# Kernel optimization log

Hardware: AMD Instinct MI355X
Metric: run time of the kernel (lower is better)

Reference implementation:

```python
import jax, jax.numpy as jnp
import numpy as np

E = 128      # embedding_dim
H = 64       # hidden_dim
B = 2048     # batch
L = 200      # history length
NEG = -1e30  # stand-in for -inf (avoids NaN for all-pad rows; same math when any key unmasked)


def setup_inputs() -> dict:
    key = jax.random.key(0)
    ks = jax.random.split(key, 10)
    s1 = 1.0 / np.sqrt(4 * E)
    s2 = 1.0 / np.sqrt(H)
    return {
        "query": jax.random.normal(ks[0], (B, E), jnp.float32),
        "keys": jax.random.normal(ks[1], (B, L, E), jnp.float32),
        "mask": jax.random.randint(ks[2], (B, L), 0, 2, jnp.int32),
        "W1": jax.random.uniform(ks[3], (4 * E, H), jnp.float32, -s1, s1),
        "b1": jax.random.uniform(ks[4], (H,), jnp.float32, -s1, s1),
        "W2": jax.random.uniform(ks[5], (H, H), jnp.float32, -s2, s2),
        "b2": jax.random.uniform(ks[6], (H,), jnp.float32, -s2, s2),
        "W3": jax.random.uniform(ks[7], (H, 1), jnp.float32, -s2, s2),
        "b3": jax.random.uniform(ks[8], (1,), jnp.float32, -s2, s2),
        "no_hist": jax.random.normal(ks[9], (E,), jnp.float32) * 0.001,
    }


def reference(query, keys, mask, W1, b1, W2, b2, W3, b3, no_hist):
    # q expanded over L, 4-way concat features: [q, k, q*k, q-k] -> (B, L, 4E)
    q = jnp.broadcast_to(query[:, None, :], keys.shape)
    attn_in = jnp.concatenate([q, keys, q * keys, q - keys], axis=-1)
    # 3-layer MLP scorer -> (B, L)
    h = jax.nn.relu(attn_in @ W1 + b1)
    h = jax.nn.relu(h @ W2 + b2)
    scores = (h @ W3 + b3)[..., 0]
    # masked softmax over L, then zero masked slots and renormalize
    m = mask.astype(scores.dtype)
    scores = jnp.where(m == 0, NEG, scores)
    attn = jax.nn.softmax(scores, axis=1) * m
    denom = jnp.sum(attn, axis=1, keepdims=True)
    attn = attn / (denom + 1e-12)
    # weighted sum of keys -> (B, E)
    user_interest = jnp.einsum("bl,ble->be", attn, keys)
    # rows with no history get the learned no-hist embedding
    all_pad = jnp.sum(m, axis=1) == 0  # (B,)
    user_interest = jnp.where(all_pad[:, None], no_hist[None, :], user_interest)
    return user_interest
```

## Files before the change

### kernel.cpp

```cpp
#include <hip/hip_runtime.h>


#define NB 2048
#define LE 128
#define LH 64
#define LL 200
#define NMT 13

typedef short bf16x8 __attribute__((ext_vector_type(8)));
typedef float f32x4 __attribute__((ext_vector_type(4)));

__device__ __forceinline__ short f2bf(float f) {
  unsigned u = __float_as_uint(f);
  u += 0x7fffu + ((u >> 16) & 1u);
  return (short)(u >> 16);
}

struct __align__(16) SM {
  short keys[208 * 128];
  short h1[4][16 * 72];
  float scores[208];
  float q[128];
  float bias1[64];
  float b2s[64];
  float w3s[64];
  float red[16];
};

__global__ void k0_prep(const float* __restrict__ W1, const float* __restrict__ W2,
                        float* __restrict__ BD, float* __restrict__ Cq,
                        float* __restrict__ AD, short* __restrict__ W2T) {
  int idx = blockIdx.x * 256 + threadIdx.x;
  if (idx < 8192) {
    int h = idx >> 7, e = idx & 127;
    BD[idx] = W1[(128 + e) * LH + h] - W1[(384 + e) * LH + h];
    Cq[idx] = W1[(256 + e) * LH + h];
    int e2 = idx >> 6, h2 = idx & 63;
    AD[idx] = W1[e2 * LH + h2] + W1[(384 + e2) * LH + h2];
    if (idx < 4096) {
      int c = idx >> 6, k = idx & 63;
      W2T[idx] = f2bf(W2[k * LH + c]);
    }
  }
}

__global__ void __launch_bounds__(256, 2)
din_attn(const float* __restrict__ query, const float* __restrict__ keysg,
         const int* __restrict__ mask, const float* __restrict__ b1,
         const float* __restrict__ b2, const float* __restrict__ W3,
         const float* __restrict__ no_hist,
         const float* __restrict__ BD, const float* __restrict__ Cq,
         const float* __restrict__ AD, const short* __restrict__ W2T,
         float* __restrict__ out)
{
  __shared__ SM sm;
  const int b    = blockIdx.x;
  const int t    = threadIdx.x;
  const int lane = t & 63;
  const int wv   = t >> 6;
  const int col  = lane & 15;
  const int quad = lane >> 4;

  int my_mask = 0;
  if (t < LL) my_mask = mask[b * LL + t];
  if (t < LE) sm.q[t] = query[b * LE + t];
  if (t < LH) { sm.b2s[t] = b2[t]; sm.w3s[t] = W3[t]; }
  __syncthreads();

  bf16x8 fB2[4][2];
  #pragma unroll
  for (int n = 0; n < 4; ++n)
    #pragma unroll
    for (int k2 = 0; k2 < 2; ++k2)
      fB2[n][k2] = *(const bf16x8*)&W2T[(n * 16 + col) * 64 + k2 * 32 + quad * 8];

  short* scratch = &sm.keys[0];
  #pragma unroll
  for (int i = 0; i < 4; ++i) {
    int idx = (t + 256 * i) * 8;
    int h = idx >> 7, e0 = idx & 127;
    float4 bd0 = *(const float4*)&BD[idx];
    float4 bd1 = *(const float4*)&BD[idx + 4];
    float4 c0  = *(const float4*)&Cq[idx];
    float4 c1  = *(const float4*)&Cq[idx + 4];
    bf16x8 w;
    w[0] = f2bf(bd0.x + sm.q[e0 + 0] * c0.x);
    w[1] = f2bf(bd0.y + sm.q[e0 + 1] * c0.y);
    w[2] = f2bf(bd0.z + sm.q[e0 + 2] * c0.z);
    w[3] = f2bf(bd0.w + sm.q[e0 + 3] * c0.w);
    w[4] = f2bf(bd1.x + sm.q[e0 + 4] * c1.x);
    w[5] = f2bf(bd1.y + sm.q[e0 + 5] * c1.y);
    w[6] = f2bf(bd1.z + sm.q[e0 + 6] * c1.z);
    w[7] = f2bf(bd1.w + sm.q[e0 + 7] * c1.w);
    *(bf16x8*)&scratch[h * 136 + e0] = w;
  }
  {
    int h = lane;
    float acc = 0.f;
    #pragma unroll 8
    for (int e = wv * 32; e < wv * 32 + 32; ++e)
      acc = fmaf(sm.q[e], AD[e * LH + h], acc);
    float* biasp = (float*)&sm.h1[0][0];
    biasp[wv * 64 + h] = acc;
  }
  __syncthreads();

  bf16x8 fB1[4][4];
  #pragma unroll
  for (int n = 0; n < 4; ++n)
    #pragma unroll
    for (int kt = 0; kt < 4; ++kt)
      fB1[n][kt] = *(const bf16x8*)&scratch[(n * 16 + col) * 136 + kt * 32 + quad * 8];

  if (t < LH) {
    const float* biasp = (const float*)&sm.h1[0][0];
    sm.bias1[t] = b1[t] + biasp[t] + biasp[64 + t] + biasp[128 + t] + biasp[192 + t];
  }
  __syncthreads();

  const float* kb = keysg + (size_t)b * LL * LE;
  short* h1w = &sm.h1[wv][0];

  auto do_tile = [&](int mt) {
    int row = mt * 16 + col;
    int rowg = row < LL ? row : LL - 1;
    const float* rp = kb + rowg * LE;
    bf16x8 a[4];
    #pragma unroll
    for (int kt = 0; kt < 4; ++kt) {
      float4 v0 = *(const float4*)&rp[kt * 32 + quad * 8];
      float4 v1 = *(const float4*)&rp[kt * 32 + quad * 8 + 4];
      bf16x8 av;
      av[0] = f2bf(v0.x); av[1] = f2bf(v0.y); av[2] = f2bf(v0.z); av[3] = f2bf(v0.w);
      av[4] = f2bf(v1.x); av[5] = f2bf(v1.y); av[6] = f2bf(v1.z); av[7] = f2bf(v1.w);
      a[kt] = av;
      *(bf16x8*)&sm.keys[row * 128 + (((kt * 4 + quad) ^ col) * 8)] = av;
    }
    #pragma unroll
    for (int n = 0; n < 4; ++n) {
      f32x4 acc = {0.f, 0.f, 0.f, 0.f};
      #pragma unroll
      for (int kt = 0; kt < 4; ++kt)
        acc = __builtin_amdgcn_mfma_f32_16x16x32_bf16(a[kt], fB1[n][kt], acc, 0, 0, 0);
      float bias = sm.bias1[n * 16 + col];
      #pragma unroll
      for (int i = 0; i < 4; ++i)
        h1w[(quad * 4 + i) * 72 + n * 16 + col] = f2bf(fmaxf(acc[i] + bias, 0.f));
    }
    bf16x8 a2[2];
    #pragma unroll
    for (int k2 = 0; k2 < 2; ++k2)
      a2[k2] = *(const bf16x8*)&h1w[col * 72 + k2 * 32 + quad * 8];
    float p[4] = {0.f, 0.f, 0.f, 0.f};
    #pragma unroll
    for (int n = 0; n < 4; ++n) {
      f32x4 c2 = {0.f, 0.f, 0.f, 0.f};
      c2 = __builtin_amdgcn_mfma_f32_16x16x32_bf16(a2[0], fB2[n][0], c2, 0, 0, 0);
      c2 = __builtin_amdgcn_mfma_f32_16x16x32_bf16(a2[1], fB2[n][1], c2, 0, 0, 0);
      float bb = sm.b2s[n * 16 + col];
      float w3 = sm.w3s[n * 16 + col];
      #pragma unroll
      for (int i = 0; i < 4; ++i)
        p[i] = fmaf(fmaxf(c2[i] + bb, 0.f), w3, p[i]);
    }
    #pragma unroll
    for (int i = 0; i < 4; ++i) {
      #pragma unroll
      for (int off = 1; off < 16; off <<= 1)
        p[i] += __shfl_xor(p[i], off);
      if (col == 0) sm.scores[mt * 16 + quad * 4 + i] = p[i];
    }
  };

  do_tile(wv);
  do_tile(wv + 4);
  do_tile(wv + 8);
  if (wv == 0) do_tile(12);
  __syncthreads();

  float sc = (t < LL) ? sm.scores[t] : -3.0e38f;
  float vmax = (my_mask != 0) ? sc : -3.0e38f;
  #pragma unroll
  for (int off = 1; off < 64; off <<= 1) vmax = fmaxf(vmax, __shfl_xor(vmax, off));
  if (lane == 0) sm.red[wv] = vmax;
  __syncthreads();
  float M = fmaxf(fmaxf(sm.red[0], sm.red[1]), fmaxf(sm.red[2], sm.red[3]));
  float ex = (t < LL && my_mask != 0) ? __expf(sc - M) : 0.f;
  float vsum = ex;
  #pragma unroll
  for (int off = 1; off < 64; off <<= 1) vsum += __shfl_xor(vsum, off);
  if (lane == 0) sm.red[4 + wv] = vsum;
  __syncthreads();
  float Z = sm.red[4] + sm.red[5] + sm.red[6] + sm.red[7];
  bool allpad = !(Z > 0.f);
  float rz = allpad ? 0.f : (1.f / Z);
  if (t < 208) sm.scores[t] = (t < LL) ? ex * rz : 0.f;
  __syncthreads();

  {
    const int part = t >> 5;
    const int ei = (t & 31) * 4;
    float a0 = 0.f, a1 = 0.f, a2s = 0.f, a3 = 0.f;
    int l0 = part * 25;
    #pragma unroll 5
    for (int li = 0; li < 25; ++li) {
      int l = l0 + li;
      float aw = sm.scores[l];
      int blk = (ei >> 3) ^ (l & 15);
      const short* kp = &sm.keys[l * 128 + blk * 8 + (ei & 7)];
      int2 kv = *(const int2*)kp;
      unsigned kx = (unsigned)kv.x, ky = (unsigned)kv.y;
      a0  = fmaf(aw, __uint_as_float(kx << 16), a0);
      a1  = fmaf(aw, __uint_as_float(kx & 0xffff0000u), a1);
      a2s = fmaf(aw, __uint_as_float(ky << 16), a2s);
      a3  = fmaf(aw, __uint_as_float(ky & 0xffff0000u), a3);
    }
    float* redf = (float*)&sm.h1[0][0];
    *(float4*)&redf[part * 128 + ei] = make_float4(a0, a1, a2s, a3);
    __syncthreads();
    if (t < LE) {
      float s = 0.f;
      #pragma unroll
      for (int pp = 0; pp < 8; ++pp) s += redf[pp * 128 + t];
      if (allpad) s = no_hist[t];
      out[b * LE + t] = s;
    }
  }
}

extern "C" void kernel_launch(void* const* d_in, const int* in_sizes, int n_in,
                              void* d_out, int out_size, void* d_ws, size_t ws_size,
                              hipStream_t stream) {
  (void)in_sizes; (void)n_in; (void)ws_size; (void)out_size;
  const float* query   = (const float*)d_in[0];
  const float* keysg   = (const float*)d_in[1];
  const int*   mask    = (const int*)d_in[2];
  const float* W1      = (const float*)d_in[3];
  const float* b1      = (const float*)d_in[4];
  const float* W2      = (const float*)d_in[5];
  const float* b2      = (const float*)d_in[6];
  const float* W3      = (const float*)d_in[7];
  const float* no_hist = (const float*)d_in[9];

  float* BD  = (float*)d_ws;
  float* Cq  = BD + 8192;
  float* AD  = Cq + 8192;
  short* W2T = (short*)(AD + 8192);

  k0_prep<<<32, 256, 0, stream>>>(W1, W2, BD, Cq, AD, W2T);
  din_attn<<<NB, 256, 0, stream>>>(query, keysg, mask, b1, b2, W3, no_hist,
                                   BD, Cq, AD, W2T, (float*)d_out);
}
```

Baseline: 327.4 us.

## Keep bf16 key tiles in registers and drop the shared-memory key buffer

Each wave now keeps its converted bf16 key A-fragments in registers and computes the weighted key sum directly from them with cross-lane shuffles. This replaces the 53KB shared keys array and the second pass that read it back. Shared memory drops to about 25KB, so the launch bound is raised to 3 blocks per CU. Other changes: the first key tile is prefetched before the weight setup, the softmax is done per wave with one fewer barrier, the mask is applied when scores are written, and biases are held in registers. The cost is more register pressure (16 bf16x8 fragments per lane), which could force spills or defeat the higher occupancy target.

```diff
diff --git a/kernel.cpp b/kernel.cpp
--- a/kernel.cpp
+++ b/kernel.cpp
@@ -5,7 +5,6 @@
 #define LE 128
 #define LH 64
 #define LL 200
-#define NMT 13
 
 typedef short bf16x8 __attribute__((ext_vector_type(8)));
 typedef float f32x4 __attribute__((ext_vector_type(4)));
@@ -15,16 +14,16 @@
   u += 0x7fffu + ((u >> 16) & 1u);
   return (short)(u >> 16);
 }
+__device__ __forceinline__ float bf2f(short h) {
+  return __uint_as_float(((unsigned)(unsigned short)h) << 16);
+}
 
 struct __align__(16) SM {
-  short keys[208 * 128];
+  short wk[64 * 136];
   short h1[4][16 * 72];
   float scores[208];
-  float q[128];
-  float bias1[64];
-  float b2s[64];
-  float w3s[64];
-  float red[16];
+  int   smask[208];
+  float biasp[4][64];
 };
 
 __global__ void k0_prep(const float* __restrict__ W1, const float* __restrict__ W2,
@@ -44,7 +43,7 @@
   }
 }
 
-__global__ void __launch_bounds__(256, 2)
+__global__ void __launch_bounds__(256, 3)
 din_attn(const float* __restrict__ query, const float* __restrict__ keysg,
          const int* __restrict__ mask, const float* __restrict__ b1,
          const float* __restrict__ b2, const float* __restrict__ W3,
@@ -61,11 +60,55 @@
   const int col  = lane & 15;
   const int quad = lane >> 4;
 
-  int my_mask = 0;
-  if (t < LL) my_mask = mask[b * LL + t];
-  if (t < LE) sm.q[t] = query[b * LE + t];
-  if (t < LH) { sm.b2s[t] = b2[t]; sm.w3s[t] = W3[t]; }
+  const float* kb = keysg + (size_t)b * (LL * LE);
+
+  float4 pre[8];
+  {
+    int row = wv * 16 + col;
+    const float* rp = kb + row * LE;
+    #pragma unroll
+    for (int kt = 0; kt < 4; ++kt) {
+      pre[2 * kt]     = *(const float4*)&rp[kt * 32 + quad * 8];
+      pre[2 * kt + 1] = *(const float4*)&rp[kt * 32 + quad * 8 + 4];
+    }
+  }
+
+  if (t < 208) sm.smask[t] = (t < LL) ? mask[b * LL + t] : 0;
+
+  {
+    const int e0 = (t * 4) & 127;
+    float4 qv = *(const float4*)&query[b * LE + e0];
+    #pragma unroll
+    for (int i = 0; i < 8; ++i) {
+      int idx = t * 4 + i * 1024;
+      int h = idx >> 7;
+      float4 bd = *(const float4*)&BD[idx];
+      float4 cq = *(const float4*)&Cq[idx];
+      short w0 = f2bf(bd.x + qv.x * cq.x);
+      short w1 = f2bf(bd.y + qv.y * cq.y);
+      short w2 = f2bf(bd.z + qv.z * cq.z);
+      short w3v = f2bf(bd.w + qv.w * cq.w);
+      short4 wq = make_short4(w0, w1, w2, w3v);
+      *(short4*)&sm.wk[h * 136 + e0] = wq;
+    }
+  }
+  {
+    float acc = 0.f;
+    const float* adp = &AD[(wv * 32) * LH + lane];
+    const float* qp  = &query[b * LE + wv * 32];
+    #pragma unroll 8
+    for (int e = 0; e < 32; ++e)
+      acc = fmaf(qp[e], adp[e * LH], acc);
+    sm.biasp[wv][lane] = acc;
+  }
   __syncthreads();
+
+  bf16x8 fB1[4][4];
+  #pragma unroll
+  for (int n = 0; n < 4; ++n)
+    #pragma unroll
+    for (int kt = 0; kt < 4; ++kt)
+      fB1[n][kt] = *(const bf16x8*)&sm.wk[(n * 16 + col) * 136 + kt * 32 + quad * 8];
 
   bf16x8 fB2[4][2];
   #pragma unroll
@@ -74,67 +117,34 @@
     for (int k2 = 0; k2 < 2; ++k2)
       fB2[n][k2] = *(const bf16x8*)&W2T[(n * 16 + col) * 64 + k2 * 32 + quad * 8];
 
-  short* scratch = &sm.keys[0];
-  #pragma unroll
-  for (int i = 0; i < 4; ++i) {
-    int idx = (t + 256 * i) * 8;
-    int h = idx >> 7, e0 = idx & 127;
-    float4 bd0 = *(const float4*)&BD[idx];
-    float4 bd1 = *(const float4*)&BD[idx + 4];
-    float4 c0  = *(const float4*)&Cq[idx];
-    float4 c1  = *(const float4*)&Cq[idx + 4];
-    bf16x8 w;
-    w[0] = f2bf(bd0.x + sm.q[e0 + 0] * c0.x);
-    w[1] = f2bf(bd0.y + sm.q[e0 + 1] * c0.y);
-    w[2] = f2bf(bd0.z + sm.q[e0 + 2] * c0.z);
-    w[3] = f2bf(bd0.w + sm.q[e0 + 3] * c0.w);
-    w[4] = f2bf(bd1.x + sm.q[e0 + 4] * c1.x);
-    w[5] = f2bf(bd1.y + sm.q[e0 + 5] * c1.y);
-    w[6] = f2bf(bd1.z + sm.q[e0 + 6] * c1.z);
-    w[7] = f2bf(bd1.w + sm.q[e0 + 7] * c1.w);
-    *(bf16x8*)&scratch[h * 136 + e0] = w;
-  }
-  {
-    int h = lane;
-    float acc = 0.f;
-    #pragma unroll 8
-    for (int e = wv * 32; e < wv * 32 + 32; ++e)
-      acc = fmaf(sm.q[e], AD[e * LH + h], acc);
-    float* biasp = (float*)&sm.h1[0][0];
-    biasp[wv * 64 + h] = acc;
-  }
-  __syncthreads();
-
-  bf16x8 fB1[4][4];
-  #pragma unroll
-  for (int n = 0; n < 4; ++n)
-    #pragma unroll
-    for (int kt = 0; kt < 4; ++kt)
-      fB1[n][kt] = *(const bf16x8*)&scratch[(n * 16 + col) * 136 + kt * 32 + quad * 8];
-
-  if (t < LH) {
-    const float* biasp = (const float*)&sm.h1[0][0];
-    sm.bias1[t] = b1[t] + biasp[t] + biasp[64 + t] + biasp[128 + t] + biasp[192 + t];
-  }
-  __syncthreads();
-
-  const float* kb = keysg + (size_t)b * LL * LE;
+  float bias1r[4], b2r[4], w3r[4];
+  #pragma unroll
+  for (int n = 0; n < 4; ++n) {
+    int h = n * 16 + col;
+    bias1r[n] = b1[h] + sm.biasp[0][h] + sm.biasp[1][h] + sm.biasp[2][h] + sm.biasp[3][h];
+    b2r[n] = b2[h];
+    w3r[n] = W3[h];
+  }
+
+  bf16x8 ak[4][4];
   short* h1w = &sm.h1[wv][0];
 
-  auto do_tile = [&](int mt) {
+  auto do_tile = [&](int mt, bf16x8 (&a)[4], const float4* preld) {
     int row = mt * 16 + col;
     int rowg = row < LL ? row : LL - 1;
     const float* rp = kb + rowg * LE;
-    bf16x8 a[4];
     #pragma unroll
     for (int kt = 0; kt < 4; ++kt) {
-      float4 v0 = *(const float4*)&rp[kt * 32 + quad * 8];
-      float4 v1 = *(const float4*)&rp[kt * 32 + quad * 8 + 4];
+      float4 v0, v1;
+      if (preld) { v0 = preld[2 * kt]; v1 = preld[2 * kt + 1]; }
+      else {
+        v0 = *(const float4*)&rp[kt * 32 + quad * 8];
+        v1 = *(const float4*)&rp[kt * 32 + quad * 8 + 4];
+      }
       bf16x8 av;
       av[0] = f2bf(v0.x); av[1] = f2bf(v0.y); av[2] = f2bf(v0.z); av[3] = f2bf(v0.w);
       av[4] = f2bf(v1.x); av[5] = f2bf(v1.y); av[6] = f2bf(v1.z); av[7] = f2bf(v1.w);
       a[kt] = av;
-      *(bf16x8*)&sm.keys[row * 128 + (((kt * 4 + quad) ^ col) * 8)] = av;
     }
     #pragma unroll
     for (int n = 0; n < 4; ++n) {
@@ -142,10 +152,10 @@
       #pragma unroll
       for (int kt = 0; kt < 4; ++kt)
         acc = __builtin_amdgcn_mfma_f32_16x16x32_bf16(a[kt], fB1[n][kt], acc, 0, 0, 0);
-      float bias = sm.bias1[n * 16 + col];
       #pragma unroll
       for (int i = 0; i < 4; ++i)
-        h1w[(quad * 4 + i) * 72 + n * 16 + col] = f2bf(fmaxf(acc[i] + bias, 0.f));
+        h1w[(quad * 4 + i) * 72 + n * 16 + col] =
+            f2bf(fmaxf(acc[i] + bias1r[n], 0.f));
     }
     bf16x8 a2[2];
     #pragma unroll
@@ -157,74 +167,86 @@
       f32x4 c2 = {0.f, 0.f, 0.f, 0.f};
       c2 = __builtin_amdgcn_mfma_f32_16x16x32_bf16(a2[0], fB2[n][0], c2, 0, 0, 0);
       c2 = __builtin_amdgcn_mfma_f32_16x16x32_bf16(a2[1], fB2[n][1], c2, 0, 0, 0);
-      float bb = sm.b2s[n * 16 + col];
-      float w3 = sm.w3s[n * 16 + col];
       #pragma unroll
       for (int i = 0; i < 4; ++i)
-        p[i] = fmaf(fmaxf(c2[i] + bb, 0.f), w3, p[i]);
+        p[i] = fmaf(fmaxf(c2[i] + b2r[n], 0.f), w3r[n], p[i]);
     }
     #pragma unroll
     for (int i = 0; i < 4; ++i) {
       #pragma unroll
       for (int off = 1; off < 16; off <<= 1)
         p[i] += __shfl_xor(p[i], off);
-      if (col == 0) sm.scores[mt * 16 + quad * 4 + i] = p[i];
+      if (col == 0) {
+        int r = mt * 16 + quad * 4 + i;
+        sm.scores[r] = sm.smask[r] ? p[i] : -3.0e38f;
+      }
     }
   };
 
-  do_tile(wv);
-  do_tile(wv + 4);
-  do_tile(wv + 8);
-  if (wv == 0) do_tile(12);
+  do_tile(wv,     ak[0], pre);
+  do_tile(wv + 4, ak[1], nullptr);
+  do_tile(wv + 8, ak[2], nullptr);
+  if (wv == 0) do_tile(12, ak[3], nullptr);
   __syncthreads();
 
-  float sc = (t < LL) ? sm.scores[t] : -3.0e38f;
-  float vmax = (my_mask != 0) ? sc : -3.0e38f;
-  #pragma unroll
-  for (int off = 1; off < 64; off <<= 1) vmax = fmaxf(vmax, __shfl_xor(vmax, off));
-  if (lane == 0) sm.red[wv] = vmax;
+  float s0 = sm.scores[lane];
+  float s1 = sm.scores[lane + 64];
+  float s2 = sm.scores[lane + 128];
+  float s3 = (lane < 16) ? sm.scores[lane + 192] : -3.0e38f;
+  float M = fmaxf(fmaxf(s0, s1), fmaxf(s2, s3));
+  #pragma unroll
+  for (int off = 1; off < 64; off <<= 1) M = fmaxf(M, __shfl_xor(M, off));
+  bool allpad = (M <= -1.0e38f);
+  float ex[4];
+  ex[0] = __expf(s0 - M);
+  ex[1] = __expf(s1 - M);
+  ex[2] = __expf(s2 - M);
+  ex[3] = (lane < 16) ? __expf(s3 - M) : 0.f;
+  float Z = ex[0] + ex[1] + ex[2] + ex[3];
+  #pragma unroll
+  for (int off = 1; off < 64; off <<= 1) Z += __shfl_xor(Z, off);
+  float rz = allpad ? 0.f : (1.f / Z);
+  ex[0] *= rz; ex[1] *= rz; ex[2] *= rz; ex[3] *= rz;
+
+  float at0 = __shfl(ex[0], wv * 16 + col);
+  float at1 = __shfl(ex[1], wv * 16 + col);
+  float at2 = __shfl(ex[2], wv * 16 + col);
+  float at3 = __shfl(ex[3], col);
+
+  float* redfw = (float*)&sm.h1[wv][0];
+  #pragma unroll
+  for (int kt = 0; kt < 4; ++kt) {
+    float acc8[8] = {0.f, 0.f, 0.f, 0.f, 0.f, 0.f, 0.f, 0.f};
+    #pragma unroll
+    for (int x = 0; x < 8; ++x) {
+      acc8[x] = fmaf(at0, bf2f(ak[0][kt][x]), acc8[x]);
+      acc8[x] = fmaf(at1, bf2f(ak[1][kt][x]), acc8[x]);
+      acc8[x] = fmaf(at2, bf2f(ak[2][kt][x]), acc8[x]);
+    }
+    if (wv == 0) {
+      #pragma unroll
+      for (int x = 0; x < 8; ++x)
+        acc8[x] = fmaf(at3, bf2f(ak[3][kt][x]), acc8[x]);
+    }
+    #pragma unroll
+    for (int off = 1; off < 16; off <<= 1)
+      #pragma unroll
+      for (int x = 0; x < 8; ++x)
+        acc8[x] += __shfl_xor(acc8[x], off);
+    if (col == 0) {
+      *(float4*)&redfw[kt * 32 + quad * 8]     =
+          make_float4(acc8[0], acc8[1], acc8[2], acc8[3]);
+      *(float4*)&redfw[kt * 32 + quad * 8 + 4] =
+          make_float4(acc8[4], acc8[5], acc8[6], acc8[7]);
+    }
+  }
   __syncthreads();
-  float M = fmaxf(fmaxf(sm.red[0], sm.red[1]), fmaxf(sm.red[2], sm.red[3]));
-  float ex = (t < LL && my_mask != 0) ? __expf(sc - M) : 0.f;
-  float vsum = ex;
-  #pragma unroll
-  for (int off = 1; off < 64; off <<= 1) vsum += __shfl_xor(vsum, off);
-  if (lane == 0) sm.red[4 + wv] = vsum;
-  __syncthreads();
-  float Z = sm.red[4] + sm.red[5] + sm.red[6] + sm.red[7];
-  bool allpad = !(Z > 0.f);
-  float rz = allpad ? 0.f : (1.f / Z);
-  if (t < 208) sm.scores[t] = (t < LL) ? ex * rz : 0.f;
-  __syncthreads();
-
-  {
-    const int part = t >> 5;
-    const int ei = (t & 31) * 4;
-    float a0 = 0.f, a1 = 0.f, a2s = 0.f, a3 = 0.f;
-    int l0 = part * 25;
-    #pragma unroll 5
-    for (int li = 0; li < 25; ++li) {
-      int l = l0 + li;
-      float aw = sm.scores[l];
-      int blk = (ei >> 3) ^ (l & 15);
-      const short* kp = &sm.keys[l * 128 + blk * 8 + (ei & 7)];
-      int2 kv = *(const int2*)kp;
-      unsigned kx = (unsigned)kv.x, ky = (unsigned)kv.y;
-      a0  = fmaf(aw, __uint_as_float(kx << 16), a0);
-      a1  = fmaf(aw, __uint_as_float(kx & 0xffff0000u), a1);
-      a2s = fmaf(aw, __uint_as_float(ky << 16), a2s);
-      a3  = fmaf(aw, __uint_as_float(ky & 0xffff0000u), a3);
-    }
-    float* redf = (float*)&sm.h1[0][0];
-    *(float4*)&redf[part * 128 + ei] = make_float4(a0, a1, a2s, a3);
-    __syncthreads();
-    if (t < LE) {
-      float s = 0.f;
-      #pragma unroll
-      for (int pp = 0; pp < 8; ++pp) s += redf[pp * 128 + t];
-      if (allpad) s = no_hist[t];
-      out[b * LE + t] = s;
-    }
+
+  if (t < LE) {
+    const float* r0 = (const float*)&sm.h1[0][0];
+    float s = r0[t] + r0[576 + t] + r0[1152 + t] + r0[1728 + t];
+    if (allpad) s = no_hist[t];
+    out[b * LE + t] = s;
   }
 }
 
```

After: 406.0 us. 1.24x slower.
